# Kernel tuning notes

Hardware: AMD Instinct MI355X
Metric: run time of the kernel (lower is better)

## Reference

```python
import jax, jax.numpy as jnp
import numpy as np

B, T, D = 1, 2048, 4096
N, K, H = 32, 8, 128  # num_heads, num_kv_heads, head_dim
ROPE_BASE = 10000
SCALE_FACTOR = 1.0
EPS = 1e-6
NEG_INF = -1e9


def rms_norm(x):
    var = jnp.mean(jnp.square(x), axis=-1, keepdims=True)
    return x * jax.lax.rsqrt(var + EPS)


def apply_rope(x, positions, base_frequency, scale_factor=1.0):
    # x: [B, L, num_heads, H], positions: [B, L]
    head_dim = x.shape[-1]
    fraction = 2.0 * jnp.arange(head_dim // 2, dtype=jnp.float32) / head_dim
    timescale = base_frequency ** fraction  # [H/2]
    sinusoid = positions[..., None].astype(jnp.float32) / timescale  # [B,L,H/2]
    sinusoid = sinusoid[..., None, :] / scale_factor  # [B,L,1,H/2]
    sin, cos = jnp.sin(sinusoid), jnp.cos(sinusoid)
    x1, x2 = jnp.split(x, 2, axis=-1)
    return jnp.concatenate([x1 * cos - x2 * sin, x2 * cos + x1 * sin], axis=-1)


def setup_inputs() -> dict:
    key = jax.random.key(0)
    ks = jax.random.split(key, 7)
    x = jax.random.normal(ks[0], (B, T, D), dtype=jnp.float32)
    segment_pos = jnp.broadcast_to(jnp.arange(T, dtype=jnp.int32)[None, :], (B, T))
    causal = jnp.tril(jnp.ones((T, T), dtype=bool))
    attn_mask = jnp.where(causal, 0.0, NEG_INF).astype(jnp.float32)[None]  # [B,T,S]
    attn_mask = jnp.broadcast_to(attn_mask, (B, T, T))
    q_w = jax.random.normal(ks[1], (N, D, H), dtype=jnp.float32) * (D ** -0.5)
    kv_w = jax.random.normal(ks[2], (2, K, D, H), dtype=jnp.float32) * (D ** -0.5)
    o_w = jax.random.normal(ks[3], (N, H, D), dtype=jnp.float32) * ((N * H) ** -0.5)
    q_scale = jax.random.normal(ks[4], (H,), dtype=jnp.float32) * 0.02  # RMSNorm scale (zeros-init style)
    k_scale = jax.random.normal(ks[5], (H,), dtype=jnp.float32) * 0.02
    return {"x": x, "segment_pos": segment_pos, "attn_mask": attn_mask,
            "q_w": q_w, "kv_w": kv_w, "o_w": o_w,
            "q_scale": q_scale, "k_scale": k_scale}


def reference(x, segment_pos, attn_mask, q_w, kv_w, o_w, q_scale, k_scale):
    # Projections
    q = jnp.einsum('BTD,NDH->BTNH', x, q_w)          # [B,T,N,H]
    kv = jnp.einsum('BSD,CKDH->CBSKH', x, kv_w)      # [2,B,S,K,H]
    k, v = kv[0], kv[1]
    # QK RMSNorm (with scale, (1+scale) convention) and value RMSNorm (no scale)
    q = rms_norm(q) * (1.0 + q_scale)
    k = rms_norm(k) * (1.0 + k_scale)
    v = rms_norm(v)
    # RoPE (standard path: positions are [B,L])
    q = apply_rope(q, segment_pos, ROPE_BASE, SCALE_FACTOR)
    k = apply_rope(k, segment_pos, ROPE_BASE, SCALE_FACTOR)
    # GQA grouping: [B,T,K,G,H]
    G = N // K
    qg = q.reshape(B, T, K, G, H)
    attn_logits = jnp.einsum('btkgh,bskh->bkgts', qg, k)  # [B,K,G,T,S]
    attn_logits = attn_logits + attn_mask[:, None, None, :, :]
    attn_weights = jax.nn.softmax(attn_logits, axis=-1).astype(v.dtype)
    out = jnp.einsum('bkgts,bskh->btkgh', attn_weights, v)  # [B,T,K,G,H]
    out = out.reshape(B, T, N, H)
    return jnp.einsum('BTNH,NHD->BTD', out, o_w)
```

## Files before the change

kernel.cpp:

```cpp
#include <hip/hip_runtime.h>
#include <stdint.h>


typedef __bf16 bf16x8 __attribute__((ext_vector_type(8)));
typedef float  f32x4  __attribute__((ext_vector_type(4)));

__device__ __forceinline__ uint16_t f2bf(float f) {
    union { float f; uint32_t u; } v; v.f = f;
    uint32_t r = v.u + 0x7fffu + ((v.u >> 16) & 1u);
    return (uint16_t)(r >> 16);
}

__device__ __forceinline__ void gload_lds16(const void* g, void* l) {
    __builtin_amdgcn_global_load_lds(
        (const __attribute__((address_space(1))) uint32_t*)g,
        (__attribute__((address_space(3))) uint32_t*)l, 16, 0, 0);
}

__global__ __launch_bounds__(256) void k_cvt_x(const float* __restrict__ x,
                                               uint16_t* __restrict__ xb) {
    int i = (blockIdx.x * 256 + threadIdx.x) * 8;
    int r = i >> 12, k = i & 4095;
    float4 a = *(const float4*)(x + i);
    float4 b = *(const float4*)(x + i + 4);
    uint16_t tmp[8];
    tmp[0] = f2bf(a.x); tmp[1] = f2bf(a.y); tmp[2] = f2bf(a.z); tmp[3] = f2bf(a.w);
    tmp[4] = f2bf(b.x); tmp[5] = f2bf(b.y); tmp[6] = f2bf(b.z); tmp[7] = f2bf(b.w);
    int dst = r * 4096 + (k & ~63) + (((((k >> 3) & 7) ^ (r & 7))) << 3);
    *(uint4*)(xb + dst) = *(uint4*)tmp;
}

__global__ __launch_bounds__(256) void k_prep_wt(const float* __restrict__ qw,
                                                 const float* __restrict__ kvw,
                                                 uint16_t* __restrict__ Wt) {
    const int hx = blockIdx.x, dx = blockIdx.y, m = blockIdx.z;
    const float* src = (m < 32) ? (qw + (size_t)m * 524288)
                                : (kvw + (size_t)(m - 32) * 524288);
    __shared__ uint16_t tile[64][65];
    const int t = threadIdx.x, d0 = dx * 64, h0 = hx * 64;
#pragma unroll
    for (int i = 0; i < 16; ++i) {
        int idx = i * 256 + t, r = idx >> 6, c = idx & 63;
        tile[r][c] = f2bf(src[(size_t)(d0 + r) * 128 + h0 + c]);
    }
    __syncthreads();
#pragma unroll
    for (int it = 0; it < 2; ++it) {
        int slot = it * 256 + t, hr = slot >> 3, cl = slot & 7;
        int R = m * 128 + h0 + hr;
        uint16_t tmp[8];
#pragma unroll
        for (int e = 0; e < 8; ++e) tmp[e] = tile[cl * 8 + e][hr];
        *(uint4*)&Wt[(size_t)R * 4096 + d0 + ((cl ^ (R & 7)) << 3)] = *(uint4*)tmp;
    }
}

__global__ __launch_bounds__(256) void k_prep_ot(const float* __restrict__ ow,
                                                 uint16_t* __restrict__ Ot) {
    const int dx = blockIdx.x, hx = blockIdx.y, n = blockIdx.z;
    const float* src = ow + (size_t)n * 524288;
    __shared__ uint16_t tile[64][65];
    const int t = threadIdx.x, h0 = hx * 64, d0 = dx * 64;
#pragma unroll
    for (int i = 0; i < 16; ++i) {
        int idx = i * 256 + t, r = idx >> 6, c = idx & 63;
        tile[r][c] = f2bf(src[(size_t)(h0 + r) * 4096 + d0 + c]);
    }
    __syncthreads();
#pragma unroll
    for (int it = 0; it < 2; ++it) {
        int slot = it * 256 + t, dr = slot >> 3, cl = slot & 7;
        int R = d0 + dr;
        uint16_t tmp[8];
#pragma unroll
        for (int e = 0; e < 8; ++e) tmp[e] = tile[cl * 8 + e][dr];
        *(uint4*)&Ot[(size_t)R * 4096 + n * 128 + h0 + ((cl ^ (R & 7)) << 3)] = *(uint4*)tmp;
    }
}

__global__ __launch_bounds__(256) void k_gemm_qkv(const uint16_t* __restrict__ A,
                                                  const uint16_t* __restrict__ Bt,
                                                  const int* __restrict__ pos,
                                                  const float* __restrict__ qs,
                                                  const float* __restrict__ ks,
                                                  uint16_t* __restrict__ Qg,
                                                  uint16_t* __restrict__ Kg,
                                                  uint16_t* __restrict__ Vg) {
    __shared__ __align__(16) char smem[33792];
    uint16_t* As  = (uint16_t*)smem;
    uint16_t* Bs  = (uint16_t*)(smem + 16384);
    float*    X   = (float*)smem;
    float*    ssq = (float*)(smem + 32768);
    const int Kd = 4096;
    const int t = threadIdx.x;
    const int wave = t >> 6, lane = t & 63, l16 = lane & 15, quad = lane >> 4;
    const int wr = wave >> 1, wc = wave & 1;
    const int n = blockIdx.x, bm0 = blockIdx.y * 128, bn0 = n * 128;
    const int sw = l16 & 7;

    f32x4 acc[4][4];
    const f32x4 z4 = {0.f, 0.f, 0.f, 0.f};
#pragma unroll
    for (int i = 0; i < 4; ++i)
#pragma unroll
        for (int j = 0; j < 4; ++j) acc[i][j] = z4;

    const size_t laneOff = (size_t)(lane >> 3) * Kd + (lane & 7) * 8;
    const uint16_t* aBase = A  + (size_t)(bm0 + wave * 32) * Kd + laneOff;
    const uint16_t* bBase = Bt + (size_t)(bn0 + wave * 32) * Kd + laneOff;

    for (int kb = 0; kb < Kd; kb += 64) {
        __syncthreads();
#pragma unroll
        for (int j = 0; j < 4; ++j) {
            gload_lds16(aBase + (size_t)j * 8 * Kd + kb, &As[(wave * 32 + j * 8) * 64]);
            gload_lds16(bBase + (size_t)j * 8 * Kd + kb, &Bs[(wave * 32 + j * 8) * 64]);
        }
        __syncthreads();
#pragma unroll
        for (int kc = 0; kc < 2; ++kc) {
            bf16x8 af[4], bf[4];
#pragma unroll
            for (int i = 0; i < 4; ++i)
                af[i] = *(const bf16x8*)&As[(wr * 64 + i * 16 + l16) * 64 + (((kc * 4 + quad) ^ sw) << 3)];
#pragma unroll
            for (int j = 0; j < 4; ++j)
                bf[j] = *(const bf16x8*)&Bs[(wc * 64 + j * 16 + l16) * 64 + (((kc * 4 + quad) ^ sw) << 3)];
#pragma unroll
            for (int i = 0; i < 4; ++i)
#pragma unroll
                for (int j = 0; j < 4; ++j)
                    acc[i][j] = __builtin_amdgcn_mfma_f32_16x16x32_bf16(af[i], bf[j], acc[i][j], 0, 0, 0);
        }
    }

#pragma unroll
    for (int i = 0; i < 4; ++i)
#pragma unroll
        for (int r = 0; r < 4; ++r) {
            float s = 0.f;
#pragma unroll
            for (int j = 0; j < 4; ++j) s += acc[i][j][r] * acc[i][j][r];
            s += __shfl_xor(s, 1); s += __shfl_xor(s, 2);
            s += __shfl_xor(s, 4); s += __shfl_xor(s, 8);
            if (l16 == 0) ssq[(wr * 64 + i * 16 + quad * 4 + r) * 2 + wc] = s;
        }
    __syncthreads();

    float s1 = 0.f, s2 = 0.f, invts = 0.f;
    if (n < 40) {
        const float* sc = (n < 32) ? qs : ks;
        s1 = 1.0f + sc[lane];
        s2 = 1.0f + sc[lane + 64];
        invts = exp2f((float)lane * -0.20762050593046014f);
    }

#pragma unroll
    for (int pass = 0; pass < 2; ++pass) {
        if (wr == pass) {
#pragma unroll
            for (int i = 0; i < 4; ++i)
#pragma unroll
                for (int j = 0; j < 4; ++j)
#pragma unroll
                    for (int r = 0; r < 4; ++r)
                        X[(i * 16 + quad * 4 + r) * 128 + wc * 64 + j * 16 + l16] = acc[i][j][r];
        }
        __syncthreads();
        for (int rr = 0; rr < 16; ++rr) {
            int lrow = wave * 16 + rr;
            int grow = bm0 + pass * 64 + lrow;
            float rn = rsqrtf((ssq[(pass * 64 + lrow) * 2] + ssq[(pass * 64 + lrow) * 2 + 1])
                              * 0.0078125f + 1e-6f);
            float x1 = X[lrow * 128 + lane];
            float x2 = X[lrow * 128 + lane + 64];
            if (n < 40) {
                float y1 = x1 * rn * s1, y2 = x2 * rn * s2;
                float ang = (float)pos[grow] * invts;
                float sn = sinf(ang), cs = cosf(ang);
                X[lrow * 128 + lane]      = y1 * cs - y2 * sn;
                X[lrow * 128 + lane + 64] = y2 * cs + y1 * sn;
            } else {
                X[lrow * 128 + lane]      = x1 * rn;
                X[lrow * 128 + lane + 64] = x2 * rn;
            }
        }
        __syncthreads();
        if (n < 40) {
#pragma unroll
            for (int it = 0; it < 4; ++it) {
                int slot = it * 256 + t, lrow = slot >> 4, c = slot & 15;
                int tg = bm0 + pass * 64 + lrow;
                f32x4 a = *(f32x4*)&X[lrow * 128 + c * 8];
                f32x4 b = *(f32x4*)&X[lrow * 128 + c * 8 + 4];
                uint16_t tmp[8];
#pragma unroll
                for (int e = 0; e < 4; ++e) { tmp[e] = f2bf(a[e]); tmp[4 + e] = f2bf(b[e]); }
                if (n < 32)
                    *(uint4*)&Qg[((size_t)n * 2048 + tg) * 128 + c * 8] = *(uint4*)tmp;
                else
                    *(uint4*)&Kg[((size_t)(n - 32) * 2048 + tg) * 128 + ((c ^ (tg & 15)) << 3)] = *(uint4*)tmp;
            }
        } else {
#pragma unroll
            for (int it = 0; it < 4; ++it) {
                int slot = it * 256 + t, h = slot >> 3, scl = slot & 7;
                int sc = pass * 8 + scl;
                uint16_t tmp[8];
#pragma unroll
                for (int e = 0; e < 8; ++e) tmp[e] = f2bf(X[(scl * 8 + e) * 128 + h]);
                *(uint4*)&Vg[((size_t)(n - 40) * 128 + h) * 2048 + bm0 + ((sc ^ (h & 15)) << 3)] = *(uint4*)tmp;
            }
        }
        __syncthreads();
    }
}

__global__ __launch_bounds__(256) void k_gemm2(const uint16_t* __restrict__ A,
                                               const uint16_t* __restrict__ Bt,
                                               float* __restrict__ C0,
                                               float* __restrict__ C1p,
                                               int M, int N, int Kd) {
    __shared__ uint16_t As[128 * 64];
    __shared__ uint16_t Bs[128 * 64];
    const int t = threadIdx.x;
    const int wave = t >> 6, lane = t & 63, l16 = lane & 15, quad = lane >> 4;
    const int wr = wave >> 1, wc = wave & 1;
    const int bm0 = blockIdx.y * 128, bn0 = blockIdx.x * 128;
    const int kz = blockIdx.z;
    const int sw = l16 & 7;
    float* C = kz ? C1p : C0;

    f32x4 acc[4][4];
    const f32x4 z4 = {0.f, 0.f, 0.f, 0.f};
#pragma unroll
    for (int i = 0; i < 4; ++i)
#pragma unroll
        for (int j = 0; j < 4; ++j) acc[i][j] = z4;

    const size_t laneOff = (size_t)(lane >> 3) * Kd + (lane & 7) * 8;
    const uint16_t* aBase = A  + (size_t)(bm0 + wave * 32) * Kd + laneOff;
    const uint16_t* bBase = Bt + (size_t)(bn0 + wave * 32) * Kd + laneOff;

    const int kbeg = kz * (Kd >> 1), kend = kbeg + (Kd >> 1);
    for (int kb = kbeg; kb < kend; kb += 64) {
        __syncthreads();
#pragma unroll
        for (int j = 0; j < 4; ++j) {
            gload_lds16(aBase + (size_t)j * 8 * Kd + kb, &As[(wave * 32 + j * 8) * 64]);
            gload_lds16(bBase + (size_t)j * 8 * Kd + kb, &Bs[(wave * 32 + j * 8) * 64]);
        }
        __syncthreads();
#pragma unroll
        for (int kc = 0; kc < 2; ++kc) {
            bf16x8 af[4], bf[4];
#pragma unroll
            for (int i = 0; i < 4; ++i)
                af[i] = *(const bf16x8*)&As[(wr * 64 + i * 16 + l16) * 64 + (((kc * 4 + quad) ^ sw) << 3)];
#pragma unroll
            for (int j = 0; j < 4; ++j)
                bf[j] = *(const bf16x8*)&Bs[(wc * 64 + j * 16 + l16) * 64 + (((kc * 4 + quad) ^ sw) << 3)];
#pragma unroll
            for (int i = 0; i < 4; ++i)
#pragma unroll
                for (int j = 0; j < 4; ++j)
                    acc[i][j] = __builtin_amdgcn_mfma_f32_16x16x32_bf16(af[i], bf[j], acc[i][j], 0, 0, 0);
        }
    }
#pragma unroll
    for (int i = 0; i < 4; ++i)
#pragma unroll
        for (int j = 0; j < 4; ++j) {
            int row = bm0 + wr * 64 + i * 16 + quad * 4;
            int col = bn0 + wc * 64 + j * 16 + l16;
            float* cp = C + (size_t)row * N + col;
            cp[0]             = acc[i][j][0];
            cp[(size_t)N]     = acc[i][j][1];
            cp[2 * (size_t)N] = acc[i][j][2];
            cp[3 * (size_t)N] = acc[i][j][3];
        }
}

__global__ __launch_bounds__(256) void k_reduce(float* __restrict__ out,
                                                const float* __restrict__ p) {
    int i = (blockIdx.x * 256 + threadIdx.x) * 4;
    float4 a = *(float4*)(out + i);
    float4 b = *(const float4*)(p + i);
    a.x += b.x; a.y += b.y; a.z += b.z; a.w += b.w;
    *(float4*)(out + i) = a;
}

__global__ __launch_bounds__(256) void k_attn(const uint16_t* __restrict__ Q,
                                              const uint16_t* __restrict__ K,
                                              const uint16_t* __restrict__ Vt,
                                              uint16_t* __restrict__ att) {
    __shared__ uint16_t sK[128 * 128];
    __shared__ uint16_t sV[128 * 128];
    const int p = blockIdx.x, n = blockIdx.y, kk = n >> 2;
    const int t = threadIdx.x, wave = t >> 6, lane = t & 63;
    const int l16 = lane & 15, quad = lane >> 4;
    const f32x4 z4 = {0.f, 0.f, 0.f, 0.f};

    const uint16_t* Kbase = K  + ((size_t)kk * 2048 + wave * 32 + (lane >> 4)) * 128 + (lane & 15) * 8;
    const uint16_t* Vbase = Vt + ((size_t)kk * 128  + wave * 32 + (lane >> 4)) * 2048 + (lane & 15) * 8;

    for (int half = 0; half < 2; ++half) {
        const int qt = half ? (31 - p) : p;
        const int q0 = qt * 64;
        const int nk = (qt >> 1) + 1;

        bf16x8 qf[4];
#pragma unroll
        for (int kc = 0; kc < 4; ++kc)
            qf[kc] = *(const bf16x8*)(Q + (size_t)(n * 2048 + q0 + wave * 16 + l16) * 128 + kc * 32 + quad * 8);

        f32x4 O[8];
#pragma unroll
        for (int h = 0; h < 8; ++h) O[h] = z4;
        float mrow[4], lrow[4];
#pragma unroll
        for (int r = 0; r < 4; ++r) { mrow[r] = -INFINITY; lrow[r] = 0.f; }

        for (int st = 0; st < nk; ++st) {
            const int s0 = st * 128;
            __syncthreads();
#pragma unroll
            for (int j = 0; j < 8; ++j) {
                gload_lds16(Kbase + (size_t)(s0 + j * 4) * 128, &sK[(wave * 32 + j * 4) * 128]);
                gload_lds16(Vbase + (size_t)j * 4 * 2048 + s0,  &sV[(wave * 32 + j * 4) * 128]);
            }
            __syncthreads();

            f32x4 S[8];
#pragma unroll
            for (int jn = 0; jn < 8; ++jn) S[jn] = z4;
#pragma unroll
            for (int jn = 0; jn < 8; ++jn) {
                int krow = jn * 16 + l16;
#pragma unroll
                for (int kc = 0; kc < 4; ++kc) {
                    bf16x8 b = *(const bf16x8*)&sK[krow * 128 + (((kc * 4 + quad) ^ l16) << 3)];
                    S[jn] = __builtin_amdgcn_mfma_f32_16x16x32_bf16(qf[kc], b, S[jn], 0, 0, 0);
                }
            }
            if (st == nk - 1) {
#pragma unroll
                for (int jn = 0; jn < 8; ++jn) {
                    int sc = s0 + jn * 16 + l16;
#pragma unroll
                    for (int r = 0; r < 4; ++r) {
                        int mr = q0 + wave * 16 + quad * 4 + r;
                        if (sc > mr) S[jn][r] = -INFINITY;
                    }
                }
            }
            float alpha[4];
#pragma unroll
            for (int r = 0; r < 4; ++r) {
                float mx = S[0][r];
#pragma unroll
                for (int jn = 1; jn < 8; ++jn) mx = fmaxf(mx, S[jn][r]);
                mx = fmaxf(mx, __shfl_xor(mx, 1));
                mx = fmaxf(mx, __shfl_xor(mx, 2));
                mx = fmaxf(mx, __shfl_xor(mx, 4));
                mx = fmaxf(mx, __shfl_xor(mx, 8));
                float mnew = fmaxf(mrow[r], mx);
                float a = __expf(mrow[r] - mnew);
                mrow[r] = mnew;
                float sum = 0.f;
#pragma unroll
                for (int jn = 0; jn < 8; ++jn) {
                    float e = __expf(S[jn][r] - mnew);
                    S[jn][r] = e;
                    sum += e;
                }
                sum += __shfl_xor(sum, 1);
                sum += __shfl_xor(sum, 2);
                sum += __shfl_xor(sum, 4);
                sum += __shfl_xor(sum, 8);
                lrow[r] = lrow[r] * a + sum;
                alpha[r] = a;
            }
#pragma unroll
            for (int h = 0; h < 8; ++h)
#pragma unroll
                for (int r = 0; r < 4; ++r) O[h][r] *= alpha[r];

            __syncthreads();
#pragma unroll
            for (int jn = 0; jn < 8; ++jn)
#pragma unroll
                for (int r = 0; r < 4; ++r) {
                    int prow = wave * 16 + quad * 4 + r;
                    int pcol = jn * 16 + l16;
                    sK[prow * 128 + ((pcol & 7) | ((((pcol >> 3) ^ prow) & 15) << 3))]
                        = f2bf(S[jn][r]);
                }
            bf16x8 pf[4];
#pragma unroll
            for (int ksv = 0; ksv < 4; ++ksv)
                pf[ksv] = *(const bf16x8*)&sK[(wave * 16 + l16) * 128 + (((ksv * 4 + quad) ^ l16) << 3)];
#pragma unroll
            for (int hj = 0; hj < 8; ++hj) {
                int vrow = hj * 16 + l16;
#pragma unroll
                for (int ksv = 0; ksv < 4; ++ksv) {
                    bf16x8 b = *(const bf16x8*)&sV[vrow * 128 + (((ksv * 4 + quad) ^ l16) << 3)];
                    O[hj] = __builtin_amdgcn_mfma_f32_16x16x32_bf16(pf[ksv], b, O[hj], 0, 0, 0);
                }
            }
        }

        __syncthreads();
        uint16_t* sO = &sK[wave * 2112];
        float inv[4];
#pragma unroll
        for (int r = 0; r < 4; ++r) inv[r] = 1.0f / lrow[r];
#pragma unroll
        for (int hj = 0; hj < 8; ++hj)
#pragma unroll
            for (int r = 0; r < 4; ++r)
                sO[(quad * 4 + r) * 132 + hj * 16 + l16] = f2bf(O[hj][r] * inv[r]);
#pragma unroll
        for (int it = 0; it < 4; ++it) {
            int slot = it * 64 + lane, rloc = slot >> 4, cl = slot & 15;
            bf16x8 v = *(const bf16x8*)&sO[rloc * 132 + cl * 8];
            int R = q0 + wave * 16 + rloc;
            size_t dst = (size_t)R * 4096 + n * 128 + ((cl & 8) << 3) + (((cl & 7) ^ (R & 7)) << 3);
            *(uint4*)&att[dst] = *(uint4*)&v;
        }
    }
}

extern "C" void kernel_launch(void* const* d_in, const int* in_sizes, int n_in,
                              void* d_out, int out_size, void* d_ws, size_t ws_size,
                              hipStream_t stream) {
    const float* x   = (const float*)d_in[0];
    const int*   sp  = (const int*)d_in[1];
    const float* qw  = (const float*)d_in[3];
    const float* kvw = (const float*)d_in[4];
    const float* ow  = (const float*)d_in[5];
    const float* qsc = (const float*)d_in[6];
    const float* ksc = (const float*)d_in[7];
    float* out = (float*)d_out;

    char* ws = (char*)d_ws;
    uint16_t* xb   = (uint16_t*)(ws);
    uint16_t* Wt   = (uint16_t*)(ws + (size_t)(16u << 20));
    uint16_t* Qb   = (uint16_t*)(ws + (size_t)(64u << 20));
    uint16_t* Kb   = (uint16_t*)(ws + (size_t)(80u << 20));
    uint16_t* Vtb  = (uint16_t*)(ws + (size_t)(84u << 20));
    uint16_t* att  = (uint16_t*)(ws);
    uint16_t* Ot   = (uint16_t*)(ws + (size_t)(16u << 20));
    float*    part = (float*)   (ws + (size_t)(48u << 20));

    k_cvt_x    <<<4096, 256, 0, stream>>>(x, xb);
    k_prep_wt  <<<dim3(2, 64, 48), 256, 0, stream>>>(qw, kvw, Wt);
    k_gemm_qkv <<<dim3(48, 16), 256, 0, stream>>>(xb, Wt, sp, qsc, ksc, Qb, Kb, Vtb);
    k_prep_ot  <<<dim3(64, 2, 32), 256, 0, stream>>>(ow, Ot);
    k_attn     <<<dim3(16, 32), 256, 0, stream>>>(Qb, Kb, Vtb, att);
    k_gemm2    <<<dim3(32, 16, 2), 256, 0, stream>>>(att, Ot, out, part, 2048, 4096, 4096);
    k_reduce   <<<8192, 256, 0, stream>>>(out, part);
}
```

Measured before the change: 583.9 us.

## Rewrite QKV GEMM with 256x256 tiles and a multi-stage LDS pipeline

The QKV projection GEMM moves from 128x128 tiles with 4 waves and a load-then-compute loop to 256x256 tiles with 8 waves. It uses a 4-slab, double-buffered global-to-LDS pipeline with explicit barriers, vmcnt waits and MFMA priority raising, so loads for the next k-slices overlap with the matrix math. The epilogue is adapted to handle two heads per block and uses __sincosf. This needs about 134 KB of dynamic LDS and issues fewer, larger blocks (192), which may leave some of the GPU's compute units idle and adds register pressure.

```diff
diff --git a/kernel.cpp b/kernel.cpp
--- a/kernel.cpp
+++ b/kernel.cpp
@@ -78,64 +78,130 @@
     }
 }
 
-__global__ __launch_bounds__(256) void k_gemm_qkv(const uint16_t* __restrict__ A,
-                                                  const uint16_t* __restrict__ Bt,
-                                                  const int* __restrict__ pos,
-                                                  const float* __restrict__ qs,
-                                                  const float* __restrict__ ks,
-                                                  uint16_t* __restrict__ Qg,
-                                                  uint16_t* __restrict__ Kg,
-                                                  uint16_t* __restrict__ Vg) {
-    __shared__ __align__(16) char smem[33792];
-    uint16_t* As  = (uint16_t*)smem;
-    uint16_t* Bs  = (uint16_t*)(smem + 16384);
-    float*    X   = (float*)smem;
-    float*    ssq = (float*)(smem + 32768);
+
+#define PH_BAR do { asm volatile("" ::: "memory"); \
+                    __builtin_amdgcn_s_barrier(); \
+                    asm volatile("" ::: "memory"); } while (0)
+#define WAIT_LGKM do { asm volatile("s_waitcnt lgkmcnt(0)" ::: "memory"); \
+                       __builtin_amdgcn_sched_barrier(0); } while (0)
+#define WAIT_VM(N) do { asm volatile("s_waitcnt vmcnt(" #N ")" ::: "memory"); \
+                        __builtin_amdgcn_sched_barrier(0); } while (0)
+
+__global__ __launch_bounds__(512, 2) void k_gemm_qkv(const uint16_t* __restrict__ A,
+                                                     const uint16_t* __restrict__ Bt,
+                                                     const int* __restrict__ pos,
+                                                     const float* __restrict__ qs,
+                                                     const float* __restrict__ ks,
+                                                     uint16_t* __restrict__ Qg,
+                                                     uint16_t* __restrict__ Kg,
+                                                     uint16_t* __restrict__ Vg) {
+    extern __shared__ __align__(16) char smem[];
+    uint16_t* lds = (uint16_t*)smem;
     const int Kd = 4096;
-    const int t = threadIdx.x;
-    const int wave = t >> 6, lane = t & 63, l16 = lane & 15, quad = lane >> 4;
-    const int wr = wave >> 1, wc = wave & 1;
-    const int n = blockIdx.x, bm0 = blockIdx.y * 128, bn0 = n * 128;
-    const int sw = l16 & 7;
-
-    f32x4 acc[4][4];
+    const int t = threadIdx.x, wid = t >> 6, lane = t & 63;
+    const int l16 = lane & 15, quad = lane >> 4;
+    const int wr = wid >> 2, wc = wid & 3;
+    const int bx = blockIdx.x, bm0 = blockIdx.y * 256, bn0 = bx * 256;
+
+    f32x4 acc[8][4];
     const f32x4 z4 = {0.f, 0.f, 0.f, 0.f};
 #pragma unroll
-    for (int i = 0; i < 4; ++i)
+    for (int i = 0; i < 8; ++i)
 #pragma unroll
         for (int j = 0; j < 4; ++j) acc[i][j] = z4;
 
-    const size_t laneOff = (size_t)(lane >> 3) * Kd + (lane & 7) * 8;
-    const uint16_t* aBase = A  + (size_t)(bm0 + wave * 32) * Kd + laneOff;
-    const uint16_t* bBase = Bt + (size_t)(bn0 + wave * 32) * Kd + laneOff;
-
-    for (int kb = 0; kb < Kd; kb += 64) {
-        __syncthreads();
-#pragma unroll
-        for (int j = 0; j < 4; ++j) {
-            gload_lds16(aBase + (size_t)j * 8 * Kd + kb, &As[(wave * 32 + j * 8) * 64]);
-            gload_lds16(bBase + (size_t)j * 8 * Kd + kb, &Bs[(wave * 32 + j * 8) * 64]);
-        }
-        __syncthreads();
-#pragma unroll
-        for (int kc = 0; kc < 2; ++kc) {
-            bf16x8 af[4], bf[4];
-#pragma unroll
-            for (int i = 0; i < 4; ++i)
-                af[i] = *(const bf16x8*)&As[(wr * 64 + i * 16 + l16) * 64 + (((kc * 4 + quad) ^ sw) << 3)];
-#pragma unroll
-            for (int j = 0; j < 4; ++j)
-                bf[j] = *(const bf16x8*)&Bs[(wc * 64 + j * 16 + l16) * 64 + (((kc * 4 + quad) ^ sw) << 3)];
-#pragma unroll
-            for (int i = 0; i < 4; ++i)
-#pragma unroll
-                for (int j = 0; j < 4; ++j)
-                    acc[i][j] = __builtin_amdgcn_mfma_f32_16x16x32_bf16(af[i], bf[j], acc[i][j], 0, 0, 0);
-        }
-    }
-
-#pragma unroll
-    for (int i = 0; i < 4; ++i)
+    const int r0 = wid * 16 + (lane >> 2), c4 = lane & 3;
+    const int sw2 = (r0 >> 1) & 3, sw7 = r0 & 7;
+    const int offK0 = (((c4 ^ sw2)) ^ sw7) * 8;
+    const int offK1 = ((4 + (c4 ^ sw2)) ^ sw7) * 8;
+    const uint16_t* pA0 = A + (size_t)(bm0 + r0) * Kd;
+    const uint16_t* pA1 = pA0 + (size_t)128 * Kd;
+    const uint16_t* pB0 = Bt + (size_t)(bn0 + r0) * Kd;
+    const uint16_t* pB1 = pB0 + (size_t)128 * Kd;
+    uint16_t* stA = lds + wid * 512;
+    uint16_t* stB = lds + 32768 + wid * 512;
+
+    const int sA = (l16 >> 1) & 3;
+    const int rdA = (wr * 128 + l16) * 32 + ((quad ^ sA) << 3);
+    const int rdB = 32768 + (wc * 64 + l16) * 32 + ((quad ^ sA) << 3);
+
+    bf16x8 af[8], bf0, bf1;
+
+#define STAGE_A(SLAB, OFF, TT) do { \
+    gload_lds16(pA0 + (size_t)(TT) * 64 + (OFF), stA + (SLAB) * 8192); \
+    gload_lds16(pA1 + (size_t)(TT) * 64 + (OFF), stA + (SLAB) * 8192 + 4096); } while (0)
+#define STAGE_B(SLAB, OFF, TT) do { \
+    gload_lds16(pB0 + (size_t)(TT) * 64 + (OFF), stB + (SLAB) * 8192); \
+    gload_lds16(pB1 + (size_t)(TT) * 64 + (OFF), stB + (SLAB) * 8192 + 4096); } while (0)
+#define LOAD_AF(SLAB) do { _Pragma("unroll") \
+    for (int i_ = 0; i_ < 8; ++i_) \
+        af[i_] = *(const bf16x8*)&lds[(SLAB) * 8192 + rdA + i_ * 512]; } while (0)
+#define LOAD_BF(SLAB, CH) do { \
+    bf0 = *(const bf16x8*)&lds[(SLAB) * 8192 + rdB + (CH) * 1024]; \
+    bf1 = *(const bf16x8*)&lds[(SLAB) * 8192 + rdB + (CH) * 1024 + 512]; } while (0)
+#define MFMA_PH(CH) do { __builtin_amdgcn_s_setprio(1); \
+    _Pragma("unroll") for (int i_ = 0; i_ < 8; ++i_) { \
+        acc[i_][2*(CH)]   = __builtin_amdgcn_mfma_f32_16x16x32_bf16(af[i_], bf0, acc[i_][2*(CH)],   0, 0, 0); \
+        acc[i_][2*(CH)+1] = __builtin_amdgcn_mfma_f32_16x16x32_bf16(af[i_], bf1, acc[i_][2*(CH)+1], 0, 0, 0); } \
+    __builtin_amdgcn_s_setprio(0); } while (0)
+
+#define TILE(TT, BUF) do { \
+     \
+    LOAD_AF(2*(BUF)); LOAD_BF(2*(BUF), 0); \
+    STAGE_A((((BUF)^1)*2+1), offK1, (TT)+1); \
+    PH_BAR; WAIT_LGKM; MFMA_PH(0); PH_BAR; \
+     \
+    LOAD_BF(2*(BUF), 1); \
+    WAIT_VM(6); \
+    STAGE_B((((BUF)^1)*2+1), offK1, (TT)+1); \
+    PH_BAR; WAIT_LGKM; MFMA_PH(1); PH_BAR; \
+     \
+    LOAD_AF(2*(BUF)+1); LOAD_BF(2*(BUF)+1, 0); \
+    STAGE_A((BUF)*2, offK0, (TT)+2); \
+    PH_BAR; WAIT_LGKM; MFMA_PH(0); PH_BAR; \
+     \
+    LOAD_BF(2*(BUF)+1, 1); \
+    WAIT_VM(6); \
+    STAGE_B((BUF)*2, offK0, (TT)+2); \
+    PH_BAR; WAIT_LGKM; MFMA_PH(1); PH_BAR; \
+} while (0)
+
+    STAGE_A(0, offK0, 0); STAGE_B(0, offK0, 0);
+    STAGE_A(1, offK1, 0); STAGE_B(1, offK1, 0);
+    STAGE_A(2, offK0, 1); STAGE_B(2, offK0, 1);
+    WAIT_VM(8);
+    PH_BAR;
+
+#pragma unroll 1
+    for (int Ti = 0; Ti < 31; ++Ti) {
+        TILE(2 * Ti, 0);
+        TILE(2 * Ti + 1, 1);
+    }
+
+    STAGE_A(3, offK1, 63); STAGE_B(3, offK1, 63);
+    WAIT_VM(0);
+    PH_BAR;
+#pragma unroll
+    for (int T = 62; T < 64; ++T) {
+        const int BUF = T & 1;
+        LOAD_AF(2*BUF);   LOAD_BF(2*BUF, 0);   PH_BAR; WAIT_LGKM; MFMA_PH(0); PH_BAR;
+        LOAD_BF(2*BUF, 1);                     PH_BAR; WAIT_LGKM; MFMA_PH(1); PH_BAR;
+        LOAD_AF(2*BUF+1); LOAD_BF(2*BUF+1, 0); PH_BAR; WAIT_LGKM; MFMA_PH(0); PH_BAR;
+        LOAD_BF(2*BUF+1, 1);                   PH_BAR; WAIT_LGKM; MFMA_PH(1); PH_BAR;
+    }
+
+#undef TILE
+#undef MFMA_PH
+#undef LOAD_BF
+#undef LOAD_AF
+#undef STAGE_B
+#undef STAGE_A
+
+    float* X   = (float*)smem;
+    float* ssq = (float*)(smem + 133120);
+
+#pragma unroll
+    for (int i = 0; i < 8; ++i)
 #pragma unroll
         for (int r = 0; r < 4; ++r) {
             float s = 0.f;
@@ -143,13 +209,15 @@
             for (int j = 0; j < 4; ++j) s += acc[i][j][r] * acc[i][j][r];
             s += __shfl_xor(s, 1); s += __shfl_xor(s, 2);
             s += __shfl_xor(s, 4); s += __shfl_xor(s, 8);
-            if (l16 == 0) ssq[(wr * 64 + i * 16 + quad * 4 + r) * 2 + wc] = s;
+            if (l16 == 0)
+                ssq[(wr * 128 + i * 16 + quad * 4 + r) * 4 + (wc >> 1) * 2 + (wc & 1)] = s;
         }
     __syncthreads();
 
+    const int cat = (bx < 16) ? 0 : (bx < 20 ? 1 : 2);
     float s1 = 0.f, s2 = 0.f, invts = 0.f;
-    if (n < 40) {
-        const float* sc = (n < 32) ? qs : ks;
+    if (cat < 2) {
+        const float* sc = cat ? ks : qs;
         s1 = 1.0f + sc[lane];
         s2 = 1.0f + sc[lane + 64];
         invts = exp2f((float)lane * -0.20762050593046014f);
@@ -159,57 +227,68 @@
     for (int pass = 0; pass < 2; ++pass) {
         if (wr == pass) {
 #pragma unroll
-            for (int i = 0; i < 4; ++i)
+            for (int i = 0; i < 8; ++i)
 #pragma unroll
                 for (int j = 0; j < 4; ++j)
 #pragma unroll
                     for (int r = 0; r < 4; ++r)
-                        X[(i * 16 + quad * 4 + r) * 128 + wc * 64 + j * 16 + l16] = acc[i][j][r];
+                        X[(i * 16 + quad * 4 + r) * 260 + wc * 64 + j * 16 + l16] = acc[i][j][r];
         }
         __syncthreads();
         for (int rr = 0; rr < 16; ++rr) {
-            int lrow = wave * 16 + rr;
-            int grow = bm0 + pass * 64 + lrow;
-            float rn = rsqrtf((ssq[(pass * 64 + lrow) * 2] + ssq[(pass * 64 + lrow) * 2 + 1])
-                              * 0.0078125f + 1e-6f);
-            float x1 = X[lrow * 128 + lane];
-            float x2 = X[lrow * 128 + lane + 64];
-            if (n < 40) {
-                float y1 = x1 * rn * s1, y2 = x2 * rn * s2;
+            const int lrow = wid * 16 + rr;
+            const int grow = bm0 + pass * 128 + lrow;
+            float sn = 0.f, cs = 0.f;
+            if (cat < 2) {
                 float ang = (float)pos[grow] * invts;
-                float sn = sinf(ang), cs = cosf(ang);
-                X[lrow * 128 + lane]      = y1 * cs - y2 * sn;
-                X[lrow * 128 + lane + 64] = y2 * cs + y1 * sn;
-            } else {
-                X[lrow * 128 + lane]      = x1 * rn;
-                X[lrow * 128 + lane + 64] = x2 * rn;
+                __sincosf(ang, &sn, &cs);
+            }
+#pragma unroll
+            for (int hh = 0; hh < 2; ++hh) {
+                const int sb = (pass * 128 + lrow) * 4 + hh * 2;
+                float rn = rsqrtf((ssq[sb] + ssq[sb + 1]) * 0.0078125f + 1e-6f);
+                float x1 = X[lrow * 260 + hh * 128 + lane];
+                float x2 = X[lrow * 260 + hh * 128 + 64 + lane];
+                if (cat < 2) {
+                    float y1 = x1 * rn * s1, y2 = x2 * rn * s2;
+                    X[lrow * 260 + hh * 128 + lane]      = y1 * cs - y2 * sn;
+                    X[lrow * 260 + hh * 128 + 64 + lane] = y2 * cs + y1 * sn;
+                } else {
+                    X[lrow * 260 + hh * 128 + lane]      = x1 * rn;
+                    X[lrow * 260 + hh * 128 + 64 + lane] = x2 * rn;
+                }
             }
         }
         __syncthreads();
-        if (n < 40) {
-#pragma unroll
-            for (int it = 0; it < 4; ++it) {
-                int slot = it * 256 + t, lrow = slot >> 4, c = slot & 15;
-                int tg = bm0 + pass * 64 + lrow;
-                f32x4 a = *(f32x4*)&X[lrow * 128 + c * 8];
-                f32x4 b = *(f32x4*)&X[lrow * 128 + c * 8 + 4];
+        if (cat == 2) {
+#pragma unroll
+            for (int it = 0; it < 8; ++it) {
+                int slot = it * 512 + t, hh = slot >> 11, rem = slot & 2047;
+                int h = rem >> 4, sc2 = rem & 15;
                 uint16_t tmp[8];
 #pragma unroll
+                for (int e = 0; e < 8; ++e)
+                    tmp[e] = f2bf(X[(sc2 * 8 + e) * 260 + hh * 128 + h]);
+                int n = bx * 2 + hh;
+                *(uint4*)&Vg[((size_t)(n - 40) * 128 + h) * 2048 + (bm0 + pass * 128)
+                             + ((sc2 ^ (h & 15)) << 3)] = *(uint4*)tmp;
+            }
+        } else {
+#pragma unroll
+            for (int it = 0; it < 8; ++it) {
+                int slot = it * 512 + t, hh = slot >> 11, rem = slot & 2047;
+                int lrow = rem >> 4, c = rem & 15;
+                int tg = bm0 + pass * 128 + lrow, n = bx * 2 + hh;
+                f32x4 a = *(f32x4*)&X[lrow * 260 + hh * 128 + c * 8];
+                f32x4 b = *(f32x4*)&X[lrow * 260 + hh * 128 + c * 8 + 4];
+                uint16_t tmp[8];
+#pragma unroll
                 for (int e = 0; e < 4; ++e) { tmp[e] = f2bf(a[e]); tmp[4 + e] = f2bf(b[e]); }
-                if (n < 32)
+                if (cat == 0)
                     *(uint4*)&Qg[((size_t)n * 2048 + tg) * 128 + c * 8] = *(uint4*)tmp;
                 else
-                    *(uint4*)&Kg[((size_t)(n - 32) * 2048 + tg) * 128 + ((c ^ (tg & 15)) << 3)] = *(uint4*)tmp;
-            }
-        } else {
-#pragma unroll
-            for (int it = 0; it < 4; ++it) {
-                int slot = it * 256 + t, h = slot >> 3, scl = slot & 7;
-                int sc = pass * 8 + scl;
-                uint16_t tmp[8];
-#pragma unroll
-                for (int e = 0; e < 8; ++e) tmp[e] = f2bf(X[(scl * 8 + e) * 128 + h]);
-                *(uint4*)&Vg[((size_t)(n - 40) * 128 + h) * 2048 + bm0 + ((sc ^ (h & 15)) << 3)] = *(uint4*)tmp;
+                    *(uint4*)&Kg[((size_t)(n - 32) * 2048 + tg) * 128
+                                 + ((c ^ (tg & 15)) << 3)] = *(uint4*)tmp;
             }
         }
         __syncthreads();
@@ -454,9 +533,16 @@
     uint16_t* Ot   = (uint16_t*)(ws + (size_t)(16u << 20));
     float*    part = (float*)   (ws + (size_t)(48u << 20));
 
+    static bool attr_done = false;
+    if (!attr_done) {
+        hipFuncSetAttribute(reinterpret_cast<const void*>(k_gemm_qkv),
+                            hipFuncAttributeMaxDynamicSharedMemorySize, 137216);
+        attr_done = true;
+    }
+
     k_cvt_x    <<<4096, 256, 0, stream>>>(x, xb);
     k_prep_wt  <<<dim3(2, 64, 48), 256, 0, stream>>>(qw, kvw, Wt);
-    k_gemm_qkv <<<dim3(48, 16), 256, 0, stream>>>(xb, Wt, sp, qsc, ksc, Qb, Kb, Vtb);
+    k_gemm_qkv <<<dim3(24, 8), 512, 137216, stream>>>(xb, Wt, sp, qsc, ksc, Qb, Kb, Vtb);
     k_prep_ot  <<<dim3(64, 2, 32), 256, 0, stream>>>(ow, Ot);
     k_attn     <<<dim3(16, 32), 256, 0, stream>>>(Qb, Kb, Vtb, att);
     k_gemm2    <<<dim3(32, 16, 2), 256, 0, stream>>>(att, Ot, out, part, 2048, 4096, 4096);
```

Result: faster. 553.3 us (-5.2%).
